# Kernel optimization log

Hardware: AMD Instinct MI355X
Metric: run time of the kernel (lower is better)

## Reference

```python
import jax, jax.numpy as jnp
import numpy as np

N = 4096
RANK = 4
B = 2048
DT = 1.0
TAU = 1.0
ALPHA = float(np.sqrt(np.pi) / 2.0)  # erf slope so phi'(0)=1


def setup_inputs() -> dict:
    key = jax.random.key(0)
    k1, k2, k3, k4, k5, k6 = jax.random.split(key, 6)
    return {
        "x_t": jax.random.normal(k1, (1, B), dtype=jnp.float32),
        "h": jax.random.normal(k2, (N, B), dtype=jnp.float32),
        "m": jax.random.normal(k3, (N, 1), dtype=jnp.float32),
        "u": jax.random.normal(k4, (N, RANK), dtype=jnp.float32),
        "v": jax.random.normal(k5, (N, RANK), dtype=jnp.float32),
        "z": jax.random.normal(k6, (N, 1), dtype=jnp.float32),
    }


def reference(x_t, h, m, u, v, z):
    # phi(h) = erf(alpha * h)
    phi_h = jax.lax.erf(ALPHA * h)                      # [N, B]
    # W @ phi_h with W = (1/N) u v^T, reassociated to exploit low rank
    # (mathematically identical to materializing W)
    wph = (u @ (v.T @ phi_h)) / N                       # [N, B]
    h_update = wph + m @ x_t                            # [N, B]
    h_new = h + (DT / TAU) * (-h + h_update)            # [N, B]
    y = (z.T @ phi_h) / N                               # [1, B]
    return (y, h_new)
```

## Files before the change

kernel.cpp:

```cpp
#include <hip/hip_runtime.h>
#include <math.h>

#define N 4096
#define B 2048
#define RANK 4
#define ALPHA 0.8862269254527580f
#define INV_N (1.0f / 4096.0f)

#define SPLITS 64
#define RPB (N / SPLITS)
#define R3 16

__global__ __launch_bounds__(256) void k_reduce_partial(
    const float* __restrict__ h, const float* __restrict__ v,
    const float* __restrict__ z, float* __restrict__ partials) {
  __shared__ float lv[RPB][RANK];
  __shared__ float lz[RPB];
  const int tid = threadIdx.x;
  const int b = blockIdx.x * 256 + tid;
  const int row0 = blockIdx.y * RPB;

  for (int i = tid; i < RPB * RANK; i += 256) {
    int r = i & (RANK - 1);
    int n = i >> 2;
    lv[n][r] = v[(size_t)(row0 + n) * RANK + r];
  }
  if (tid < RPB) lz[tid] = z[row0 + tid];
  __syncthreads();

  float a0 = 0.f, a1 = 0.f, a2 = 0.f, a3 = 0.f, az = 0.f;
  const float* hp = h + (size_t)row0 * B + b;
#pragma unroll 4
  for (int i = 0; i < RPB; ++i) {
    float phi = erff(ALPHA * hp[(size_t)i * B]);
    a0 = fmaf(lv[i][0], phi, a0);
    a1 = fmaf(lv[i][1], phi, a1);
    a2 = fmaf(lv[i][2], phi, a2);
    a3 = fmaf(lv[i][3], phi, a3);
    az = fmaf(lz[i], phi, az);
  }

  float* pp = partials + ((size_t)blockIdx.y * 5) * B + b;
  pp[0 * B] = a0;
  pp[1 * B] = a1;
  pp[2 * B] = a2;
  pp[3 * B] = a3;
  pp[4 * B] = az;
}

__global__ __launch_bounds__(256) void k_reduce_final(
    const float* __restrict__ partials, float* __restrict__ sfin,
    float* __restrict__ y) {
  const int o = blockIdx.x * 256 + threadIdx.x;
  const int r = o / B;
  const int b = o - r * B;
  float s = 0.f;
#pragma unroll 8
  for (int sp = 0; sp < SPLITS; ++sp)
    s += partials[((size_t)sp * 5 + r) * B + b];
  if (r < RANK)
    sfin[(size_t)r * B + b] = s;
  else
    y[b] = s * INV_N;
}

__global__ __launch_bounds__(256) void k_update(
    const float* __restrict__ sfin, const float* __restrict__ u,
    const float* __restrict__ m, const float* __restrict__ x,
    float* __restrict__ hnew) {
  const int b4 = (blockIdx.x * 256 + threadIdx.x) * 4;
  const int row0 = blockIdx.y * R3;

  const float4 s0 = *(const float4*)(sfin + 0 * B + b4);
  const float4 s1 = *(const float4*)(sfin + 1 * B + b4);
  const float4 s2 = *(const float4*)(sfin + 2 * B + b4);
  const float4 s3 = *(const float4*)(sfin + 3 * B + b4);
  const float4 xv = *(const float4*)(x + b4);

#pragma unroll
  for (int i = 0; i < R3; ++i) {
    const int n = row0 + i;
    const float4 uv = *(const float4*)(u + (size_t)n * RANK);
    const float mv = m[n];
    float4 o;
    o.x = fmaf(mv, xv.x,
               (s0.x * uv.x + s1.x * uv.y + s2.x * uv.z + s3.x * uv.w) * INV_N);
    o.y = fmaf(mv, xv.y,
               (s0.y * uv.x + s1.y * uv.y + s2.y * uv.z + s3.y * uv.w) * INV_N);
    o.z = fmaf(mv, xv.z,
               (s0.z * uv.x + s1.z * uv.y + s2.z * uv.z + s3.z * uv.w) * INV_N);
    o.w = fmaf(mv, xv.w,
               (s0.w * uv.x + s1.w * uv.y + s2.w * uv.z + s3.w * uv.w) * INV_N);
    *(float4*)(hnew + (size_t)n * B + b4) = o;
  }
}

extern "C" void kernel_launch(void* const* d_in, const int* in_sizes, int n_in,
                              void* d_out, int out_size, void* d_ws,
                              size_t ws_size, hipStream_t stream) {
  const float* x = (const float*)d_in[0];
  const float* h = (const float*)d_in[1];
  const float* m = (const float*)d_in[2];
  const float* u = (const float*)d_in[3];
  const float* v = (const float*)d_in[4];
  const float* z = (const float*)d_in[5];

  float* y = (float*)d_out;
  float* hnew = (float*)d_out + B;

  float* partials = (float*)d_ws;
  float* sfin = (float*)d_ws + (size_t)SPLITS * 5 * B;

  k_reduce_partial<<<dim3(B / 256, SPLITS), 256, 0, stream>>>(h, v, z,
                                                              partials);
  k_reduce_final<<<(5 * B) / 256, 256, 0, stream>>>(partials, sfin, y);
  k_update<<<dim3(B / 1024, N / R3), 256, 0, stream>>>(sfin, u, m, x, hnew);
}
```

Baseline: 123.4 us.

## Vectorize reduction with float4 row-tiles and use 1D grids for partial and update kernels

The partial-reduction kernel now gives each block 8 full rows of h and has threads load float4 across both column halves. The update kernel now processes 16 rows across the full width with float4 pairs per thread. The aim is wider memory accesses and fewer, larger blocks. In exchange, the number of splits rises from 64 to 512, so the partials buffer grows roughly eightfold. That adds substantial extra write and read traffic in the final reduction and needs a larger workspace.

```diff
diff --git a/kernel.cpp b/kernel.cpp
--- a/kernel.cpp
+++ b/kernel.cpp
@@ -7,45 +7,70 @@
 #define ALPHA 0.8862269254527580f
 #define INV_N (1.0f / 4096.0f)
 
-#define SPLITS 64
-#define RPB (N / SPLITS)
-#define R3 16
+#define RPB1 8
+#define SPLITS1 (N / RPB1)
+#define RPB3 16
 
 __global__ __launch_bounds__(256) void k_reduce_partial(
     const float* __restrict__ h, const float* __restrict__ v,
     const float* __restrict__ z, float* __restrict__ partials) {
-  __shared__ float lv[RPB][RANK];
-  __shared__ float lz[RPB];
+  __shared__ float lv[RPB1 * RANK];
+  __shared__ float lz[RPB1];
   const int tid = threadIdx.x;
-  const int b = blockIdx.x * 256 + tid;
-  const int row0 = blockIdx.y * RPB;
+  const int row0 = blockIdx.x * RPB1;
 
-  for (int i = tid; i < RPB * RANK; i += 256) {
-    int r = i & (RANK - 1);
-    int n = i >> 2;
-    lv[n][r] = v[(size_t)(row0 + n) * RANK + r];
+  if (tid < RPB1 * RANK) {
+    lv[tid] = v[row0 * RANK + tid];
+  } else if (tid < RPB1 * RANK + RPB1) {
+    lz[tid - RPB1 * RANK] = z[row0 + (tid - RPB1 * RANK)];
   }
-  if (tid < RPB) lz[tid] = z[row0 + tid];
   __syncthreads();
 
-  float a0 = 0.f, a1 = 0.f, a2 = 0.f, a3 = 0.f, az = 0.f;
-  const float* hp = h + (size_t)row0 * B + b;
-#pragma unroll 4
-  for (int i = 0; i < RPB; ++i) {
-    float phi = erff(ALPHA * hp[(size_t)i * B]);
-    a0 = fmaf(lv[i][0], phi, a0);
-    a1 = fmaf(lv[i][1], phi, a1);
-    a2 = fmaf(lv[i][2], phi, a2);
-    a3 = fmaf(lv[i][3], phi, a3);
-    az = fmaf(lz[i], phi, az);
+  float4 zero = {0.f, 0.f, 0.f, 0.f};
+  float4 aA[5] = {zero, zero, zero, zero, zero};
+  float4 aB[5] = {zero, zero, zero, zero, zero};
+
+  const float* hp = h + (size_t)row0 * B + tid * 4;
+#pragma unroll
+  for (int r = 0; r < RPB1; ++r) {
+    const float4 h0 = *(const float4*)(hp + (size_t)(2 * r) * 1024);
+    const float4 h1 = *(const float4*)(hp + (size_t)(2 * r + 1) * 1024);
+    float4 p0, p1;
+    p0.x = erff(ALPHA * h0.x); p0.y = erff(ALPHA * h0.y);
+    p0.z = erff(ALPHA * h0.z); p0.w = erff(ALPHA * h0.w);
+    p1.x = erff(ALPHA * h1.x); p1.y = erff(ALPHA * h1.y);
+    p1.z = erff(ALPHA * h1.z); p1.w = erff(ALPHA * h1.w);
+    const float v0 = lv[r * 4 + 0], v1 = lv[r * 4 + 1];
+    const float v2 = lv[r * 4 + 2], v3 = lv[r * 4 + 3];
+    const float zr = lz[r];
+    aA[0].x = fmaf(v0, p0.x, aA[0].x); aA[0].y = fmaf(v0, p0.y, aA[0].y);
+    aA[0].z = fmaf(v0, p0.z, aA[0].z); aA[0].w = fmaf(v0, p0.w, aA[0].w);
+    aA[1].x = fmaf(v1, p0.x, aA[1].x); aA[1].y = fmaf(v1, p0.y, aA[1].y);
+    aA[1].z = fmaf(v1, p0.z, aA[1].z); aA[1].w = fmaf(v1, p0.w, aA[1].w);
+    aA[2].x = fmaf(v2, p0.x, aA[2].x); aA[2].y = fmaf(v2, p0.y, aA[2].y);
+    aA[2].z = fmaf(v2, p0.z, aA[2].z); aA[2].w = fmaf(v2, p0.w, aA[2].w);
+    aA[3].x = fmaf(v3, p0.x, aA[3].x); aA[3].y = fmaf(v3, p0.y, aA[3].y);
+    aA[3].z = fmaf(v3, p0.z, aA[3].z); aA[3].w = fmaf(v3, p0.w, aA[3].w);
+    aA[4].x = fmaf(zr, p0.x, aA[4].x); aA[4].y = fmaf(zr, p0.y, aA[4].y);
+    aA[4].z = fmaf(zr, p0.z, aA[4].z); aA[4].w = fmaf(zr, p0.w, aA[4].w);
+    aB[0].x = fmaf(v0, p1.x, aB[0].x); aB[0].y = fmaf(v0, p1.y, aB[0].y);
+    aB[0].z = fmaf(v0, p1.z, aB[0].z); aB[0].w = fmaf(v0, p1.w, aB[0].w);
+    aB[1].x = fmaf(v1, p1.x, aB[1].x); aB[1].y = fmaf(v1, p1.y, aB[1].y);
+    aB[1].z = fmaf(v1, p1.z, aB[1].z); aB[1].w = fmaf(v1, p1.w, aB[1].w);
+    aB[2].x = fmaf(v2, p1.x, aB[2].x); aB[2].y = fmaf(v2, p1.y, aB[2].y);
+    aB[2].z = fmaf(v2, p1.z, aB[2].z); aB[2].w = fmaf(v2, p1.w, aB[2].w);
+    aB[3].x = fmaf(v3, p1.x, aB[3].x); aB[3].y = fmaf(v3, p1.y, aB[3].y);
+    aB[3].z = fmaf(v3, p1.z, aB[3].z); aB[3].w = fmaf(v3, p1.w, aB[3].w);
+    aB[4].x = fmaf(zr, p1.x, aB[4].x); aB[4].y = fmaf(zr, p1.y, aB[4].y);
+    aB[4].z = fmaf(zr, p1.z, aB[4].z); aB[4].w = fmaf(zr, p1.w, aB[4].w);
   }
 
-  float* pp = partials + ((size_t)blockIdx.y * 5) * B + b;
-  pp[0 * B] = a0;
-  pp[1 * B] = a1;
-  pp[2 * B] = a2;
-  pp[3 * B] = a3;
-  pp[4 * B] = az;
+  float* pp = partials + (size_t)blockIdx.x * 5 * B + tid * 4;
+#pragma unroll
+  for (int r = 0; r < 5; ++r) {
+    *(float4*)(pp + (size_t)r * B) = aA[r];
+    *(float4*)(pp + (size_t)r * B + 1024) = aB[r];
+  }
 }
 
 __global__ __launch_bounds__(256) void k_reduce_final(
@@ -55,8 +80,8 @@
   const int r = o / B;
   const int b = o - r * B;
   float s = 0.f;
-#pragma unroll 8
-  for (int sp = 0; sp < SPLITS; ++sp)
+#pragma unroll 16
+  for (int sp = 0; sp < SPLITS1; ++sp)
     s += partials[((size_t)sp * 5 + r) * B + b];
   if (r < RANK)
     sfin[(size_t)r * B + b] = s;
@@ -68,30 +93,46 @@
     const float* __restrict__ sfin, const float* __restrict__ u,
     const float* __restrict__ m, const float* __restrict__ x,
     float* __restrict__ hnew) {
-  const int b4 = (blockIdx.x * 256 + threadIdx.x) * 4;
-  const int row0 = blockIdx.y * R3;
+  const int tid = threadIdx.x;
+  const int row0 = blockIdx.x * RPB3;
+  const int c0 = tid * 4;
 
-  const float4 s0 = *(const float4*)(sfin + 0 * B + b4);
-  const float4 s1 = *(const float4*)(sfin + 1 * B + b4);
-  const float4 s2 = *(const float4*)(sfin + 2 * B + b4);
-  const float4 s3 = *(const float4*)(sfin + 3 * B + b4);
-  const float4 xv = *(const float4*)(x + b4);
+  const float4 sA0 = *(const float4*)(sfin + 0 * B + c0);
+  const float4 sA1 = *(const float4*)(sfin + 1 * B + c0);
+  const float4 sA2 = *(const float4*)(sfin + 2 * B + c0);
+  const float4 sA3 = *(const float4*)(sfin + 3 * B + c0);
+  const float4 xa  = *(const float4*)(x + c0);
+  const float4 sB0 = *(const float4*)(sfin + 0 * B + c0 + 1024);
+  const float4 sB1 = *(const float4*)(sfin + 1 * B + c0 + 1024);
+  const float4 sB2 = *(const float4*)(sfin + 2 * B + c0 + 1024);
+  const float4 sB3 = *(const float4*)(sfin + 3 * B + c0 + 1024);
+  const float4 xb  = *(const float4*)(x + c0 + 1024);
 
+  float* op = hnew + (size_t)row0 * B + c0;
 #pragma unroll
-  for (int i = 0; i < R3; ++i) {
+  for (int i = 0; i < RPB3; ++i) {
     const int n = row0 + i;
     const float4 uv = *(const float4*)(u + (size_t)n * RANK);
     const float mv = m[n];
-    float4 o;
-    o.x = fmaf(mv, xv.x,
-               (s0.x * uv.x + s1.x * uv.y + s2.x * uv.z + s3.x * uv.w) * INV_N);
-    o.y = fmaf(mv, xv.y,
-               (s0.y * uv.x + s1.y * uv.y + s2.y * uv.z + s3.y * uv.w) * INV_N);
-    o.z = fmaf(mv, xv.z,
-               (s0.z * uv.x + s1.z * uv.y + s2.z * uv.z + s3.z * uv.w) * INV_N);
-    o.w = fmaf(mv, xv.w,
-               (s0.w * uv.x + s1.w * uv.y + s2.w * uv.z + s3.w * uv.w) * INV_N);
-    *(float4*)(hnew + (size_t)n * B + b4) = o;
+    float4 oA, oB;
+    oA.x = fmaf(mv, xa.x,
+                (sA0.x * uv.x + sA1.x * uv.y + sA2.x * uv.z + sA3.x * uv.w) * INV_N);
+    oA.y = fmaf(mv, xa.y,
+                (sA0.y * uv.x + sA1.y * uv.y + sA2.y * uv.z + sA3.y * uv.w) * INV_N);
+    oA.z = fmaf(mv, xa.z,
+                (sA0.z * uv.x + sA1.z * uv.y + sA2.z * uv.z + sA3.z * uv.w) * INV_N);
+    oA.w = fmaf(mv, xa.w,
+                (sA0.w * uv.x + sA1.w * uv.y + sA2.w * uv.z + sA3.w * uv.w) * INV_N);
+    oB.x = fmaf(mv, xb.x,
+                (sB0.x * uv.x + sB1.x * uv.y + sB2.x * uv.z + sB3.x * uv.w) * INV_N);
+    oB.y = fmaf(mv, xb.y,
+                (sB0.y * uv.x + sB1.y * uv.y + sB2.y * uv.z + sB3.y * uv.w) * INV_N);
+    oB.z = fmaf(mv, xb.z,
+                (sB0.z * uv.x + sB1.z * uv.y + sB2.z * uv.z + sB3.z * uv.w) * INV_N);
+    oB.w = fmaf(mv, xb.w,
+                (sB0.w * uv.x + sB1.w * uv.y + sB2.w * uv.z + sB3.w * uv.w) * INV_N);
+    *(float4*)(op + (size_t)i * B) = oA;
+    *(float4*)(op + (size_t)i * B + 1024) = oB;
   }
 }
 
@@ -109,10 +150,9 @@
   float* hnew = (float*)d_out + B;
 
   float* partials = (float*)d_ws;
-  float* sfin = (float*)d_ws + (size_t)SPLITS * 5 * B;
+  float* sfin = (float*)d_ws + (size_t)SPLITS1 * 5 * B;
 
-  k_reduce_partial<<<dim3(B / 256, SPLITS), 256, 0, stream>>>(h, v, z,
-                                                              partials);
+  k_reduce_partial<<<SPLITS1, 256, 0, stream>>>(h, v, z, partials);
   k_reduce_final<<<(5 * B) / 256, 256, 0, stream>>>(partials, sfin, y);
-  k_update<<<dim3(B / 1024, N / R3), 256, 0, stream>>>(sfin, u, m, x, hnew);
+  k_update<<<N / RPB3, 256, 0, stream>>>(sfin, u, m, x, hnew);
 }
```

Measured after the change: 132.8 us. +7.6%, slower.
